# Kernel optimization log

Measured on AMD Instinct MI355X. Metric: run time of the kernel, lower is better.

## Reference

```python
import jax, jax.numpy as jnp
import numpy as np

D_TEXT, D_AUDIO, D_HID = 1024, 768, 1024
EPS = 1e-5


def layer_norm(x, gamma, beta):
    mu = jnp.mean(x, axis=-1, keepdims=True)
    var = jnp.mean(jnp.square(x - mu), axis=-1, keepdims=True)
    return (x - mu) * jax.lax.rsqrt(var + EPS) * gamma + beta


def setup_inputs() -> dict:
    key = jax.random.key(0)
    ks = jax.random.split(key, 8)
    B, L, S = 16, 1024, 2048
    # xavier_uniform bound = sqrt(6/(fan_in+fan_out))
    def xavier(k, shape):
        bound = np.sqrt(6.0 / (shape[0] + shape[1]))
        return jax.random.uniform(k, shape, jnp.float32, -bound, bound)
    return {
        "H_l": jax.random.normal(ks[0], (B, L, D_TEXT), jnp.float32),
        "H_a": jax.random.normal(ks[1], (B, S, D_AUDIO), jnp.float32),
        "W_text": xavier(ks[2], (D_TEXT, D_HID)),
        "b_text": jnp.zeros((D_HID,), jnp.float32),
        "W_audio": xavier(ks[3], (D_AUDIO, D_HID)),
        "b_audio": jnp.zeros((D_HID,), jnp.float32),
        "W_out": xavier(ks[4], (D_HID, D_HID)),
        "b_out": jnp.zeros((D_HID,), jnp.float32),
        "g1": jnp.ones((D_HID,), jnp.float32),
        "beta1": jnp.zeros((D_HID,), jnp.float32),
        "g2": jnp.ones((D_HID,), jnp.float32),
        "beta2": jnp.zeros((D_HID,), jnp.float32),
        "g_out": jnp.ones((D_HID,), jnp.float32),
        "beta_out": jnp.zeros((D_HID,), jnp.float32),
    }


def reference(H_l, H_a, W_text, b_text, W_audio, b_audio, W_out, b_out,
              g1, beta1, g2, beta2, g_out, beta_out):
    # projections
    text_p = jnp.einsum('bld,dh->blh', H_l, W_text) + b_text    # [B,L,H]
    audio_p = jnp.einsum('bsd,dh->bsh', H_a, W_audio) + b_audio  # [B,S,H]
    Q = layer_norm(text_p, g1, beta1)
    K = layer_norm(audio_p, g2, beta2)
    V = audio_p
    scale = 1.0 / np.sqrt(D_HID).astype(np.float32)
    scores = jnp.einsum('blh,bsh->bls', Q, K) * scale            # [B,L,S]
    alpha = jax.nn.softmax(scores, axis=-1)
    # dropout is identity in eval mode
    H_hyper = jnp.einsum('bls,bsh->blh', alpha, V)               # [B,L,H]
    H_hyper = jnp.einsum('blh,hk->blk', H_hyper, W_out) + b_out
    return layer_norm(H_hyper + H_l, g_out, beta_out)
```

## Files before the change

kernel.cpp:

```cpp
#include <hip/hip_runtime.h>
#include <cstdio>

typedef unsigned short u16;
typedef __bf16 bf16x8 __attribute__((ext_vector_type(8)));
typedef float f32x4 __attribute__((ext_vector_type(4)));
typedef unsigned short us4 __attribute__((ext_vector_type(4)));
typedef unsigned short us8 __attribute__((ext_vector_type(8)));

__device__ __forceinline__ u16 f2bf(float f) {
    union { float f; unsigned u; } x; x.f = f;
    unsigned u = x.u + 0x7fffu + ((x.u >> 16) & 1u);
    return (u16)(u >> 16);
}
__device__ __forceinline__ float bf2f(u16 u) {
    union { unsigned u; float f; } x; x.u = ((unsigned)u) << 16;
    return x.f;
}


#define LDFRAG(base, row, koff) \
  (*(const bf16x8*)((const char*)(base) + (size_t)(row) * 128 + \
                    ((koff) ^ (((row) & 7) << 4))))

template<int TAG, bool HAS_BIAS, bool HAS_RESID, bool OUT_BF16, bool EMIT_VT>
__global__ __launch_bounds__(512, 2)
void gemm_nt(const u16* __restrict__ A, const u16* __restrict__ Bm,
             void* __restrict__ Cm, const float* __restrict__ bias,
             const float* __restrict__ resid, u16* __restrict__ vt,
             int K, int lda, int ldb, int ldc,
             long sA, long sB, long sC, float scale)
{
    __shared__ __align__(16) u16 lA[2 * 256 * 64];
    __shared__ __align__(16) u16 lB[2 * 256 * 64];

    const int tid = threadIdx.x;

    const int gx = gridDim.x, gy = gridDim.y;
    int flat = ((int)blockIdx.z * gy + blockIdx.y) * gx + blockIdx.x;
    const int nwg = gx * gy * (int)gridDim.z;
    const int q = nwg >> 3;
    flat = (flat & 7) * q + (flat >> 3);
    const int bx = flat % gx;
    const int t2 = flat / gx;
    const int by = t2 % gy;
    const long bz = t2 / gy;

    A  += bz * sA;
    Bm += bz * sB;
    const long cbase = bz * sC;
    const int m0 = by * 256;
    const int n0 = bx * 256;

    const int lane = tid & 63;
    const int w  = tid >> 6;
    const int wr = w >> 2, wc = w & 3;
    const int fr = lane & 15;
    const int kg = lane >> 4;

    auto stage_half = [&](int d_, int kt, int op, int h) {
        const u16* src = op ? Bm : A;
        const int  ld  = op ? ldb : lda;
        const int  bs  = op ? n0 : m0;
        u16* lds = (op ? lB : lA) + d_ * 16384 + h * 8192;
#pragma unroll
        for (int i2 = 0; i2 < 2; ++i2) {
            const int c  = i2 * 512 + tid;
            const int r  = c >> 3;
            const int kb = ((c & 7) * 16) ^ ((r & 7) << 4);
            const u16* g = src + (size_t)(bs + h * 128 + r) * ld + kt * 64 + (kb >> 1);
            __builtin_amdgcn_global_load_lds(
                (const __attribute__((address_space(1))) void*)g,
                (__attribute__((address_space(3))) void*)(lds + (size_t)c * 8), 16, 0, 0);
        }
    };
    auto stage_tile = [&](int d_, int kt) {
        stage_half(d_, kt, 0, 0); stage_half(d_, kt, 0, 1);
        stage_half(d_, kt, 1, 0); stage_half(d_, kt, 1, 1);
    };

    f32x4 acc[8][4] = {};

    const int nt = K >> 6;
    stage_tile(0, 0);

    for (int T = 0; T < nt; ++T) {
        const int d = T & 1;
        const u16* pA = lA + d * 16384;
        const u16* pB = lB + d * 16384;

        if (T + 1 < nt) {
            stage_tile(d ^ 1, T + 1);
            asm volatile("s_waitcnt vmcnt(8)" ::: "memory");
        } else {
            asm volatile("s_waitcnt vmcnt(0)" ::: "memory");
        }
        __builtin_amdgcn_s_barrier();
        asm volatile("" ::: "memory");

        bf16x8 af0[4][2], af1[4][2], bfr0[2][2], bfr1[2][2];
#pragma unroll
        for (int j = 0; j < 4; ++j)
#pragma unroll
            for (int ks = 0; ks < 2; ++ks)
                af0[j][ks] = LDFRAG(pA, wr * 128 + j * 16 + fr, ks * 64 + kg * 16);
#pragma unroll
        for (int i = 0; i < 2; ++i)
#pragma unroll
            for (int ks = 0; ks < 2; ++ks)
                bfr0[i][ks] = LDFRAG(pB, wc * 64 + i * 16 + fr, ks * 64 + kg * 16);
#pragma unroll
        for (int i = 0; i < 2; ++i)
#pragma unroll
            for (int ks = 0; ks < 2; ++ks)
                bfr1[i][ks] = LDFRAG(pB, wc * 64 + 32 + i * 16 + fr, ks * 64 + kg * 16);
#pragma unroll
        for (int j = 0; j < 4; ++j)
#pragma unroll
            for (int ks = 0; ks < 2; ++ks)
                af1[j][ks] = LDFRAG(pA, wr * 128 + 64 + j * 16 + fr, ks * 64 + kg * 16);

        __builtin_amdgcn_s_setprio(1);
#pragma unroll
        for (int j = 0; j < 4; ++j)
#pragma unroll
            for (int i = 0; i < 2; ++i)
#pragma unroll
                for (int ks = 0; ks < 2; ++ks)
                    acc[j][i] = __builtin_amdgcn_mfma_f32_16x16x32_bf16(
                        af0[j][ks], bfr0[i][ks], acc[j][i], 0, 0, 0);
#pragma unroll
        for (int j = 0; j < 4; ++j)
#pragma unroll
            for (int i = 0; i < 2; ++i)
#pragma unroll
                for (int ks = 0; ks < 2; ++ks)
                    acc[j][2 + i] = __builtin_amdgcn_mfma_f32_16x16x32_bf16(
                        af0[j][ks], bfr1[i][ks], acc[j][2 + i], 0, 0, 0);
#pragma unroll
        for (int j = 0; j < 4; ++j)
#pragma unroll
            for (int i = 0; i < 2; ++i)
#pragma unroll
                for (int ks = 0; ks < 2; ++ks)
                    acc[4 + j][i] = __builtin_amdgcn_mfma_f32_16x16x32_bf16(
                        af1[j][ks], bfr0[i][ks], acc[4 + j][i], 0, 0, 0);
#pragma unroll
        for (int j = 0; j < 4; ++j)
#pragma unroll
            for (int i = 0; i < 2; ++i)
#pragma unroll
                for (int ks = 0; ks < 2; ++ks)
                    acc[4 + j][2 + i] = __builtin_amdgcn_mfma_f32_16x16x32_bf16(
                        af1[j][ks], bfr1[i][ks], acc[4 + j][2 + i], 0, 0, 0);
        __builtin_amdgcn_s_setprio(0);

        asm volatile("" ::: "memory");
        __builtin_amdgcn_s_barrier();
        asm volatile("" ::: "memory");
    }

    const int orow = m0 + wr * 128 + kg * 4;
    const int ocol = n0 + wc * 64 + fr;
#pragma unroll
    for (int mf = 0; mf < 8; ++mf) {
        const int mbase = orow + mf * 16;
#pragma unroll
        for (int nf = 0; nf < 4; ++nf) {
            const int n = ocol + nf * 16;
            float v4[4];
#pragma unroll
            for (int r = 0; r < 4; ++r) {
                const int m = mbase + r;
                float v = acc[mf][nf][r] * scale;
                if (HAS_BIAS)  v += bias[n];
                if (HAS_RESID) v += resid[cbase + (long)m * ldc + n];
                v4[r] = v;
                if (OUT_BF16)  ((u16*)Cm)[cbase + (long)m * ldc + n] = f2bf(v);
                else           ((float*)Cm)[cbase + (long)m * ldc + n] = v;
            }
            if (EMIT_VT) {
                const long b_ = mbase >> 11;
                const int  s  = mbase & 2047;
                us4 o;
#pragma unroll
                for (int r = 0; r < 4; ++r) o[r] = f2bf(v4[r]);
                *(us4*)(vt + (b_ * 1024 + n) * 2048 + s) = o;
            }
        }
    }
}

template<bool IN_BF16, bool OUT_BF16>
__global__ __launch_bounds__(256)
void ln1024(const void* in, const float* __restrict__ g,
            const float* __restrict__ beta, void* out)
{
    const long row = blockIdx.x;
    const int tid = threadIdx.x;
    float x0, x1, x2, x3;
    if (IN_BF16) {
        const us4 v = ((const us4*)in)[row * 256 + tid];
        x0 = bf2f(v[0]); x1 = bf2f(v[1]); x2 = bf2f(v[2]); x3 = bf2f(v[3]);
    } else {
        const float4 v = ((const float4*)in)[row * 256 + tid];
        x0 = v.x; x1 = v.y; x2 = v.z; x3 = v.w;
    }
    float s  = x0 + x1 + x2 + x3;
    float s2 = x0 * x0 + x1 * x1 + x2 * x2 + x3 * x3;
#pragma unroll
    for (int off = 32; off > 0; off >>= 1) {
        s  += __shfl_xor(s, off);
        s2 += __shfl_xor(s2, off);
    }
    __shared__ float rs[4], rq[4];
    if ((tid & 63) == 0) { rs[tid >> 6] = s; rq[tid >> 6] = s2; }
    __syncthreads();
    const float S  = rs[0] + rs[1] + rs[2] + rs[3];
    const float S2 = rq[0] + rq[1] + rq[2] + rq[3];
    const float mu = S * (1.0f / 1024.0f);
    const float var = S2 * (1.0f / 1024.0f) - mu * mu;
    const float rstd = rsqrtf(var + 1e-5f);
    const float4 gg = ((const float4*)g)[tid];
    const float4 bb = ((const float4*)beta)[tid];
    const float y0 = (x0 - mu) * rstd * gg.x + bb.x;
    const float y1 = (x1 - mu) * rstd * gg.y + bb.y;
    const float y2 = (x2 - mu) * rstd * gg.z + bb.z;
    const float y3 = (x3 - mu) * rstd * gg.w + bb.w;
    if (OUT_BF16) {
        us4 o; o[0] = f2bf(y0); o[1] = f2bf(y1); o[2] = f2bf(y2); o[3] = f2bf(y3);
        ((us4*)out)[row * 256 + tid] = o;
    } else {
        float4 o; o.x = y0; o.y = y1; o.z = y2; o.w = y3;
        ((float4*)out)[row * 256 + tid] = o;
    }
}

__global__ __launch_bounds__(256)
void softmax2048_bf16(u16* io)
{
    const long row = blockIdx.x;
    const int tid = threadIdx.x;
    const us8 v = ((const us8*)io)[row * 256 + tid];
    float x[8];
#pragma unroll
    for (int i = 0; i < 8; ++i) x[i] = bf2f(v[i]);
    float m = x[0];
#pragma unroll
    for (int i = 1; i < 8; ++i) m = fmaxf(m, x[i]);
#pragma unroll
    for (int off = 32; off > 0; off >>= 1) m = fmaxf(m, __shfl_xor(m, off));
    __shared__ float rm[4], rsum[4];
    if ((tid & 63) == 0) rm[tid >> 6] = m;
    __syncthreads();
    m = fmaxf(fmaxf(rm[0], rm[1]), fmaxf(rm[2], rm[3]));
    float e[8];
    float s = 0.f;
#pragma unroll
    for (int i = 0; i < 8; ++i) { e[i] = __expf(x[i] - m); s += e[i]; }
#pragma unroll
    for (int off = 32; off > 0; off >>= 1) s += __shfl_xor(s, off);
    if ((tid & 63) == 0) rsum[tid >> 6] = s;
    __syncthreads();
    s = rsum[0] + rsum[1] + rsum[2] + rsum[3];
    const float inv = 1.0f / s;
    us8 o;
#pragma unroll
    for (int i = 0; i < 8; ++i) o[i] = f2bf(e[i] * inv);
    ((us8*)io)[row * 256 + tid] = o;
}

__global__ __launch_bounds__(256)
void cast_f32_bf16(const float* __restrict__ in, u16* __restrict__ out, long n8)
{
    const long i = (long)blockIdx.x * 256 + threadIdx.x;
    if (i >= n8) return;
    const float4 a = ((const float4*)in)[i * 2];
    const float4 b = ((const float4*)in)[i * 2 + 1];
    us8 o;
    o[0] = f2bf(a.x); o[1] = f2bf(a.y); o[2] = f2bf(a.z); o[3] = f2bf(a.w);
    o[4] = f2bf(b.x); o[5] = f2bf(b.y); o[6] = f2bf(b.z); o[7] = f2bf(b.w);
    ((us8*)out)[i] = o;
}

__global__ __launch_bounds__(256)
void tcast_f32_bf16(const float* __restrict__ in, u16* __restrict__ out,
                    int R, int C)
{
    __shared__ float t[32][33];
    const int tx = threadIdx.x, ty = threadIdx.y;
    const int c0 = blockIdx.x * 32, r0 = blockIdx.y * 32;
#pragma unroll
    for (int i = 0; i < 4; ++i)
        t[ty + i * 8][tx] = in[(long)(r0 + ty + i * 8) * C + c0 + tx];
    __syncthreads();
#pragma unroll
    for (int i = 0; i < 4; ++i)
        out[(long)(c0 + ty + i * 8) * R + r0 + tx] = f2bf(t[tx][ty + i * 8]);
}

extern "C" void kernel_launch(void* const* d_in, const int* in_sizes, int n_in,
                              void* d_out, int out_size, void* d_ws, size_t ws_size,
                              hipStream_t stream)
{
    const float* H_l      = (const float*)d_in[0];
    const float* H_a      = (const float*)d_in[1];
    const float* W_text   = (const float*)d_in[2];
    const float* b_text   = (const float*)d_in[3];
    const float* W_audio  = (const float*)d_in[4];
    const float* b_audio  = (const float*)d_in[5];
    const float* W_out    = (const float*)d_in[6];
    const float* b_out    = (const float*)d_in[7];
    const float* g1       = (const float*)d_in[8];
    const float* beta1    = (const float*)d_in[9];
    const float* g2       = (const float*)d_in[10];
    const float* beta2    = (const float*)d_in[11];
    const float* g_out    = (const float*)d_in[12];
    const float* beta_out = (const float*)d_in[13];
    (void)in_sizes; (void)n_in; (void)out_size;

    const int B = 16, L = 1024, S = 2048, DT = 1024, DA = 768, H = 1024;

    char* ws = (char*)d_ws;
    const size_t SZ_HLB = (size_t)B * L * DT * 2;
    const size_t SZ_HAB = (size_t)B * S * DA * 2;
    const size_t O_A    = SZ_HLB + SZ_HAB;
    const size_t SZ_A   = (size_t)B * L * H * 2;
    const size_t O_C    = O_A + SZ_A;
    const size_t SZ_C   = (size_t)B * S * H * 2;
    const size_t O_D    = O_C + SZ_C;
    const size_t SZ_D   = (size_t)B * S * H * 2;
    const size_t O_W    = O_D + SZ_D;
    const size_t need   = O_W + (size_t)(DT * H + DA * H + H * H) * 2;

    if (ws_size < need) {
        fprintf(stderr, "[kernel_launch] ws_size=%zu < needed=%zu — aborting launches\n",
                ws_size, need);
        return;
    }

    u16*   Hlb     = (u16*)(ws);
    u16*   Hab     = (u16*)(ws + SZ_HLB);
    u16*   Scores  = (u16*)(ws);
    u16*   Abuf    = (u16*)(ws + O_A);
    u16*   Vbuf    = (u16*)(ws + O_C);
    u16*   Kbuf    = (u16*)(ws + O_D);
    u16*   OutPre  = (u16*)(ws + O_D);
    u16*   Wt_text  = (u16*)(ws + O_W);
    u16*   Wt_audio = Wt_text + (size_t)DT * H;
    u16*   Wt_out   = Wt_audio + (size_t)DA * H;
    u16*   Vt      = (u16*)d_out;

    const float scale = 0.03125f;

    cast_f32_bf16<<<(B * L * DT / 8 + 255) / 256, 256, 0, stream>>>(H_l, Hlb, (long)B * L * DT / 8);
    cast_f32_bf16<<<(B * S * DA / 8 + 255) / 256, 256, 0, stream>>>(H_a, Hab, (long)B * S * DA / 8);
    tcast_f32_bf16<<<dim3(H / 32, DT / 32), dim3(32, 8), 0, stream>>>(W_text, Wt_text, DT, H);
    tcast_f32_bf16<<<dim3(H / 32, DA / 32), dim3(32, 8), 0, stream>>>(W_audio, Wt_audio, DA, H);
    tcast_f32_bf16<<<dim3(H / 32, H / 32),  dim3(32, 8), 0, stream>>>(W_out, Wt_out, H, H);

    gemm_nt<1, true, false, true, false><<<dim3(H / 256, B * L / 256, 1), 512, 0, stream>>>(
        Hlb, Wt_text, Abuf, b_text, nullptr, nullptr, DT, DT, DT, H, 0, 0, 0, 1.0f);
    ln1024<true, true><<<B * L, 256, 0, stream>>>(Abuf, g1, beta1, Abuf);

    gemm_nt<2, true, false, true, true><<<dim3(H / 256, B * S / 256, 1), 512, 0, stream>>>(
        Hab, Wt_audio, Vbuf, b_audio, nullptr, Vt, DA, DA, DA, H, 0, 0, 0, 1.0f);
    ln1024<true, true><<<B * S, 256, 0, stream>>>(Vbuf, g2, beta2, Kbuf);

    gemm_nt<3, false, false, true, false><<<dim3(S / 256, L / 256, B), 512, 0, stream>>>(
        Abuf, Kbuf, Scores, nullptr, nullptr, nullptr, H, H, H, S,
        (long)L * H, (long)S * H, (long)L * S, scale);

    softmax2048_bf16<<<B * L, 256, 0, stream>>>(Scores);

    gemm_nt<5, false, false, true, false><<<dim3(H / 256, L / 256, B), 512, 0, stream>>>(
        Scores, Vt, Abuf, nullptr, nullptr, nullptr, S, S, S, H,
        (long)L * S, (long)H * S, (long)L * H, 1.0f);

    gemm_nt<6, true, true, true, false><<<dim3(H / 256, B * L / 256, 1), 512, 0, stream>>>(
        Abuf, Wt_out, OutPre, b_out, H_l, nullptr, H, H, H, H, 0, 0, 0, 1.0f);

    ln1024<true, false><<<B * L, 256, 0, stream>>>(OutPre, g_out, beta_out, (float*)d_out);
}
```

Baseline: 494.4 us.

## Pipeline GEMM with a 4-slot LDS half-tile ring and interleaved prefetch

Replaces the double-buffered 256x64 LDS tiles with a four-slot ring of 128-row half-tiles and raises the prefetch distance to two K-steps. The main loop is split into four barrier-separated MFMA phases, and the global-to-LDS loads for tile T+2 are issued between phases once each half-tile is no longer being read. The goal is to hide global load latency more fully and to interleave LDS fragment reads with MFMA work across waves. The cost is eight workgroup barriers per K-step instead of two, plus more complex slot indexing that must stay race-free.

New measurement: 476.5 us. 1.04x faster.

```diff
diff --git a/kernel.cpp b/kernel.cpp
--- a/kernel.cpp
+++ b/kernel.cpp
@@ -21,6 +21,22 @@
 #define LDFRAG(base, row, koff) \
   (*(const bf16x8*)((const char*)(base) + (size_t)(row) * 128 + \
                     ((koff) ^ (((row) & 7) << 4))))
+
+#define BAR() do { \
+  asm volatile("" ::: "memory"); \
+  __builtin_amdgcn_s_barrier(); \
+  asm volatile("" ::: "memory"); \
+} while (0)
+
+#define MFMA16(AF, BF, MO, NO) do { \
+  __builtin_amdgcn_s_setprio(1); \
+  _Pragma("unroll") for (int j = 0; j < 4; ++j) \
+    _Pragma("unroll") for (int i = 0; i < 2; ++i) \
+      _Pragma("unroll") for (int ks = 0; ks < 2; ++ks) \
+        acc[(MO) + j][(NO) + i] = __builtin_amdgcn_mfma_f32_16x16x32_bf16( \
+            AF[j][ks], BF[i][ks], acc[(MO) + j][(NO) + i], 0, 0, 0); \
+  __builtin_amdgcn_s_setprio(0); \
+} while (0)
 
 template<int TAG, bool HAS_BIAS, bool HAS_RESID, bool OUT_BF16, bool EMIT_VT>
 __global__ __launch_bounds__(512, 2)
@@ -30,8 +46,8 @@
              int K, int lda, int ldb, int ldc,
              long sA, long sB, long sC, float scale)
 {
-    __shared__ __align__(16) u16 lA[2 * 256 * 64];
-    __shared__ __align__(16) u16 lB[2 * 256 * 64];
+    __shared__ __align__(16) u16 lA[4 * 128 * 64];
+    __shared__ __align__(16) u16 lB[4 * 128 * 64];
 
     const int tid = threadIdx.x;
 
@@ -57,11 +73,11 @@
     const int fr = lane & 15;
     const int kg = lane >> 4;
 
-    auto stage_half = [&](int d_, int kt, int op, int h) {
+    auto stage_half = [&](int kt, int op, int h) {
         const u16* src = op ? Bm : A;
         const int  ld  = op ? ldb : lda;
         const int  bs  = op ? n0 : m0;
-        u16* lds = (op ? lB : lA) + d_ * 16384 + h * 8192;
+        u16* lds = (op ? lB : lA) + (size_t)(((2 * kt + h) & 3)) * 8192;
 #pragma unroll
         for (int i2 = 0; i2 < 2; ++i2) {
             const int c  = i2 * 512 + tid;
@@ -73,90 +89,67 @@
                 (__attribute__((address_space(3))) void*)(lds + (size_t)c * 8), 16, 0, 0);
         }
     };
-    auto stage_tile = [&](int d_, int kt) {
-        stage_half(d_, kt, 0, 0); stage_half(d_, kt, 0, 1);
-        stage_half(d_, kt, 1, 0); stage_half(d_, kt, 1, 1);
+    auto stage_tile = [&](int kt) {
+        stage_half(kt, 0, 0); stage_half(kt, 0, 1);
+        stage_half(kt, 1, 0); stage_half(kt, 1, 1);
     };
 
     f32x4 acc[8][4] = {};
 
     const int nt = K >> 6;
-    stage_tile(0, 0);
+    stage_tile(0);
+    stage_tile(1);
+
+    const int bRowBase = (wc & 1) * 64;
 
     for (int T = 0; T < nt; ++T) {
-        const int d = T & 1;
-        const u16* pA = lA + d * 16384;
-        const u16* pB = lB + d * 16384;
-
-        if (T + 1 < nt) {
-            stage_tile(d ^ 1, T + 1);
-            asm volatile("s_waitcnt vmcnt(8)" ::: "memory");
-        } else {
-            asm volatile("s_waitcnt vmcnt(0)" ::: "memory");
-        }
-        __builtin_amdgcn_s_barrier();
-        asm volatile("" ::: "memory");
+        if (T == nt - 1) asm volatile("s_waitcnt vmcnt(0)" ::: "memory");
+        else             asm volatile("s_waitcnt vmcnt(8)" ::: "memory");
+        BAR();
+
+        const u16* pA = lA + (size_t)(((2 * T + wr) & 3)) * 8192;
+        const u16* pB = lB + (size_t)(((2 * T + (wc >> 1)) & 3)) * 8192;
+        const bool pre = (T + 2 < nt);
 
         bf16x8 af0[4][2], af1[4][2], bfr0[2][2], bfr1[2][2];
+
 #pragma unroll
         for (int j = 0; j < 4; ++j)
 #pragma unroll
             for (int ks = 0; ks < 2; ++ks)
-                af0[j][ks] = LDFRAG(pA, wr * 128 + j * 16 + fr, ks * 64 + kg * 16);
+                af0[j][ks] = LDFRAG(pA, j * 16 + fr, ks * 64 + kg * 16);
 #pragma unroll
         for (int i = 0; i < 2; ++i)
 #pragma unroll
             for (int ks = 0; ks < 2; ++ks)
-                bfr0[i][ks] = LDFRAG(pB, wc * 64 + i * 16 + fr, ks * 64 + kg * 16);
+                bfr0[i][ks] = LDFRAG(pB, bRowBase + i * 16 + fr, ks * 64 + kg * 16);
+        BAR();
+        MFMA16(af0, bfr0, 0, 0);
+        BAR();
+
 #pragma unroll
         for (int i = 0; i < 2; ++i)
 #pragma unroll
             for (int ks = 0; ks < 2; ++ks)
-                bfr1[i][ks] = LDFRAG(pB, wc * 64 + 32 + i * 16 + fr, ks * 64 + kg * 16);
+                bfr1[i][ks] = LDFRAG(pB, bRowBase + 32 + i * 16 + fr, ks * 64 + kg * 16);
+        BAR();
+        MFMA16(af0, bfr1, 0, 2);
+        BAR();
+
 #pragma unroll
         for (int j = 0; j < 4; ++j)
 #pragma unroll
             for (int ks = 0; ks < 2; ++ks)
-                af1[j][ks] = LDFRAG(pA, wr * 128 + 64 + j * 16 + fr, ks * 64 + kg * 16);
-
-        __builtin_amdgcn_s_setprio(1);
-#pragma unroll
-        for (int j = 0; j < 4; ++j)
-#pragma unroll
-            for (int i = 0; i < 2; ++i)
-#pragma unroll
-                for (int ks = 0; ks < 2; ++ks)
-                    acc[j][i] = __builtin_amdgcn_mfma_f32_16x16x32_bf16(
-                        af0[j][ks], bfr0[i][ks], acc[j][i], 0, 0, 0);
-#pragma unroll
-        for (int j = 0; j < 4; ++j)
-#pragma unroll
-            for (int i = 0; i < 2; ++i)
-#pragma unroll
-                for (int ks = 0; ks < 2; ++ks)
-                    acc[j][2 + i] = __builtin_amdgcn_mfma_f32_16x16x32_bf16(
-                        af0[j][ks], bfr1[i][ks], acc[j][2 + i], 0, 0, 0);
-#pragma unroll
-        for (int j = 0; j < 4; ++j)
-#pragma unroll
-            for (int i = 0; i < 2; ++i)
-#pragma unroll
-                for (int ks = 0; ks < 2; ++ks)
-                    acc[4 + j][i] = __builtin_amdgcn_mfma_f32_16x16x32_bf16(
-                        af1[j][ks], bfr0[i][ks], acc[4 + j][i], 0, 0, 0);
-#pragma unroll
-        for (int j = 0; j < 4; ++j)
-#pragma unroll
-            for (int i = 0; i < 2; ++i)
-#pragma unroll
-                for (int ks = 0; ks < 2; ++ks)
-                    acc[4 + j][2 + i] = __builtin_amdgcn_mfma_f32_16x16x32_bf16(
-                        af1[j][ks], bfr1[i][ks], acc[4 + j][2 + i], 0, 0, 0);
-        __builtin_amdgcn_s_setprio(0);
-
-        asm volatile("" ::: "memory");
-        __builtin_amdgcn_s_barrier();
-        asm volatile("" ::: "memory");
+                af1[j][ks] = LDFRAG(pA, 64 + j * 16 + fr, ks * 64 + kg * 16);
+        if (pre) { stage_half(T + 2, 1, 0); stage_half(T + 2, 1, 1); }
+        BAR();
+        MFMA16(af1, bfr0, 4, 0);
+        BAR();
+
+        if (pre) { stage_half(T + 2, 0, 0); stage_half(T + 2, 0, 1); }
+        BAR();
+        MFMA16(af1, bfr1, 4, 2);
+        BAR();
     }
 
     const int orow = m0 + wr * 128 + kg * 4;
```
